# Optimization experiments

Hardware: AMD Instinct MI355X
Metric: run time of the kernel (lower is better)

Reference implementation:

```python
import jax, jax.numpy as jnp
import numpy as np

HEADS = 8
K = 3            # kernel_size per axis
RPB = 2 * K - 1  # rel-pos-bias extent per axis
EPS = 1e-5


def _nbr(dim, k):
    # NATTEN-style clamped window: shift window to stay fully inside [0, dim)
    q = jnp.arange(dim)
    start = jnp.clip(q - k // 2, 0, dim - k)
    nbr = start[:, None] + jnp.arange(k)[None, :]       # (dim, k) neighbor coords
    rel = nbr - q[:, None] + (k - 1)                    # (dim, k) in [0, 2k-2]
    return nbr, rel


def _instance_norm(x):
    # InstanceNorm3d, affine=False: normalize over spatial dims per (B, C)
    m = jnp.mean(x, axis=(2, 3, 4), keepdims=True)
    v = jnp.var(x, axis=(2, 3, 4), keepdims=True)
    return (x - m) * jax.lax.rsqrt(v + EPS)


def setup_inputs() -> dict:
    key = jax.random.key(0)
    ks = jax.random.split(key, 10)
    B, C, H, W, Z = 1, 128, 32, 32, 32
    Cf = 4 * C
    s = 0.02
    return {
        "x": jax.random.normal(ks[0], (B, C, H, W, Z), jnp.float32),
        "w_qkv": jax.random.normal(ks[1], (3 * C, C), jnp.float32) * s,
        "b_qkv": jnp.zeros((3 * C,), jnp.float32),
        "rpb": jax.random.normal(ks[2], (HEADS, RPB, RPB, RPB), jnp.float32) * s,
        "w_proj": jax.random.normal(ks[3], (C, C), jnp.float32) * s,
        "b_proj": jnp.zeros((C,), jnp.float32),
        "w_ffn1": jax.random.normal(ks[4], (Cf, C), jnp.float32) * s,
        "b_ffn1": jnp.zeros((Cf,), jnp.float32),
        "w_ffn2": jax.random.normal(ks[5], (C, Cf), jnp.float32) * s,
        "b_ffn2": jnp.zeros((C,), jnp.float32),
    }


def reference(x, w_qkv, b_qkv, rpb, w_proj, b_proj, w_ffn1, b_ffn1, w_ffn2, b_ffn2):
    B, C, H, W, Z = x.shape
    hd = C // HEADS
    N = H * W * Z
    KK = K ** 3

    # ---- SAM: 3D neighborhood self-attention ----
    xt = x.reshape(B, C, N).transpose(0, 2, 1)                 # (B, N, C)
    qkv = xt @ w_qkv.T + b_qkv                                  # (B, N, 3C)
    q, k_, v = jnp.split(qkv, 3, axis=-1)
    split = lambda t: t.reshape(B, N, HEADS, hd).transpose(0, 2, 1, 3)  # (B, h, N, d)
    q, k_, v = split(q), split(k_), split(v)

    nh, rh = _nbr(H, K)
    nw, rw = _nbr(W, K)
    nz, rz = _nbr(Z, K)
    # flat neighbor token index per (h, w, z, kh, kw, kz)
    nbr = ((nh[:, None, None, :, None, None] * W
            + nw[None, :, None, None, :, None]) * Z
           + nz[None, None, :, None, None, :]).reshape(N, KK)   # (N, 27)
    # flat rel-pos-bias index
    bidx = ((rh[:, None, None, :, None, None] * RPB
             + rw[None, :, None, None, :, None]) * RPB
            + rz[None, None, :, None, None, :]).reshape(N, KK)  # (N, 27)

    kg = k_[:, :, nbr]                                          # (B, h, N, 27, d)
    vg = v[:, :, nbr]                                           # (B, h, N, 27, d)
    bias = rpb.reshape(HEADS, RPB ** 3)[:, bidx]                # (h, N, 27)

    scale = jnp.asarray(hd, x.dtype) ** -0.5
    attn = jnp.einsum('bhnd,bhnkd->bhnk', q * scale, kg) + bias
    attn = jax.nn.softmax(attn, axis=-1)
    out = jnp.einsum('bhnk,bhnkd->bhnd', attn, vg)              # (B, h, N, d)
    out = out.transpose(0, 2, 1, 3).reshape(B, N, C) @ w_proj.T + b_proj
    x5 = out.transpose(0, 2, 1).reshape(B, C, H, W, Z)

    # ---- norm_in ----
    x5 = _instance_norm(x5)

    # ---- FFN (mmcv-style, GELU, residual identity) ----
    t = x5.reshape(B, C, N).transpose(0, 2, 1)                  # (B, N, C)
    t = t + (jax.nn.gelu(t @ w_ffn1.T + b_ffn1) @ w_ffn2.T + b_ffn2)
    x5 = t.transpose(0, 2, 1).reshape(B, C, H, W, Z)

    # ---- norm_out ----
    return _instance_norm(x5)
```

## Files before the change

kernel.cpp:

```cpp
#include <hip/hip_runtime.h>
#include <hip/hip_bf16.h>
#include <math.h>

#define NPOS 32768
#define CCH  128
#define C3   384
#define CF   512

typedef __attribute__((ext_vector_type(8))) short short8;
typedef __attribute__((ext_vector_type(4))) float f32x4;

__device__ inline float bf2f(unsigned short u) {
    union { unsigned int i; float f; } x; x.i = ((unsigned int)u) << 16; return x.f;
}
__device__ inline unsigned short f2bf(float f) {
    union { float f; unsigned int i; } x; x.f = f;
    unsigned int r = x.i + 0x7FFFu + ((x.i >> 16) & 1u);
    return (unsigned short)(r >> 16);
}
__device__ inline float lo_bf(unsigned int u) {
    union { unsigned int i; float f; } x; x.i = u << 16; return x.f;
}
__device__ inline float hi_bf(unsigned int u) {
    union { unsigned int i; float f; } x; x.i = u & 0xffff0000u; return x.f;
}

template<bool GELU, bool RES, bool WF32, bool WBF>
__global__ __launch_bounds__(256) void gemm_mfma(
    const unsigned short* __restrict__ A, const unsigned short* __restrict__ B,
    const float* __restrict__ bias, const unsigned short* __restrict__ res,
    float* __restrict__ outf, unsigned short* __restrict__ outb,
    int M, int Nout, int K)
{
    __shared__ alignas(16) unsigned short As[128 * 40];
    __shared__ alignas(16) unsigned short Bs[128 * 40];

    const int tid  = threadIdx.x;
    const int lane = tid & 63;
    const int wave = tid >> 6;
    const int wm = wave & 1, wn = wave >> 1;
    const int row0 = blockIdx.y * 128;
    const int col0 = blockIdx.x * 128;

    const f32x4 fzero = {0.f, 0.f, 0.f, 0.f};
    f32x4 acc[4][4];
    #pragma unroll
    for (int i = 0; i < 4; ++i)
        #pragma unroll
        for (int j = 0; j < 4; ++j) acc[i][j] = fzero;

    const int lr = lane & 15;
    const int lk = (lane >> 4) * 8;

    for (int kt = 0; kt < K; kt += 32) {
        #pragma unroll
        for (int it = 0; it < 2; ++it) {
            const int c = tid + it * 256;
            const int r = c >> 2;
            const int p = (c & 3) * 8;
            *(uint4*)&As[r * 40 + p] = *(const uint4*)&A[(size_t)(row0 + r) * K + kt + p];
            *(uint4*)&Bs[r * 40 + p] = *(const uint4*)&B[(size_t)(col0 + r) * K + kt + p];
        }
        __syncthreads();
        short8 af[4], bfr[4];
        #pragma unroll
        for (int i = 0; i < 4; ++i)
            af[i]  = *(const short8*)&As[(wm * 64 + i * 16 + lr) * 40 + lk];
        #pragma unroll
        for (int j = 0; j < 4; ++j)
            bfr[j] = *(const short8*)&Bs[(wn * 64 + j * 16 + lr) * 40 + lk];
        #pragma unroll
        for (int i = 0; i < 4; ++i)
            #pragma unroll
            for (int j = 0; j < 4; ++j)
                acc[i][j] = __builtin_amdgcn_mfma_f32_16x16x32_bf16(
                                af[i], bfr[j], acc[i][j], 0, 0, 0);
        __syncthreads();
    }

    const int gr0 = row0 + wm * 64 + (lane >> 4) * 4;
    const int gc0 = col0 + wn * 64 + lr;
    #pragma unroll
    for (int j = 0; j < 4; ++j) {
        const int gc = gc0 + j * 16;
        const float bv = bias[gc];
        #pragma unroll
        for (int i = 0; i < 4; ++i) {
            #pragma unroll
            for (int r = 0; r < 4; ++r) {
                const int gr = gr0 + i * 16 + r;
                float v = acc[i][j][r] + bv;
                if (GELU) {
                    const float g = 0.7978845608028654f * (v + 0.044715f * v * v * v);
                    const float e = __expf(2.f * g);
                    v = v * (e / (e + 1.f));
                }
                if (RES)  v += bf2f(res[(size_t)gr * Nout + gc]);
                if (WF32) outf[(size_t)gr * Nout + gc] = v;
                if (WBF)  outb[(size_t)gr * Nout + gc] = f2bf(v);
            }
        }
    }
}

__global__ __launch_bounds__(256) void attn_tiled(
    const unsigned short* __restrict__ qkv, const float* __restrict__ rpb,
    unsigned short* __restrict__ out)
{
    __shared__ unsigned int ksu[288 * 8];
    __shared__ unsigned int vsu[288 * 8];
    __shared__ unsigned int qsu[32 * 8];
    __shared__ float logits[32 * 29];
    __shared__ float rpbs[125];

    const int t  = threadIdx.x;
    const int line = ((blockIdx.x & 7) << 7) + (blockIdx.x >> 3);
    const int h  = blockIdx.y;
    const int w0 = line & 31, h0 = line >> 5;
    const int n0 = (h0 << 10) + (w0 << 5);
    const int sh0 = min(max(h0 - 1, 0), 29);
    const int sw0 = min(max(w0 - 1, 0), 29);
    const int rh_off = sh0 - h0 + 2;
    const int rw_off = sw0 - w0 + 2;

    if (t < 64) {
        const int pos = t >> 1, part = t & 1;
        const uint4 raw = *(const uint4*)&qkv[(size_t)(n0 + pos) * C3 + h * 16 + part * 8];
        *(uint4*)&qsu[pos * 8 + part * 4] = raw;
    } else if (t < 192) {
        const int i = t - 64;
        if (i < 125) rpbs[i] = rpb[h * 125 + i];
    }
    for (int c = t; c < 1152; c += 256) {
        const int p = c >> 2, part = c & 3;
        const int ihw = p >> 5, z = p & 31;
        const int ih = (ihw * 11) >> 5;
        const int iw = ihw - 3 * ih;
        const int n = ((sh0 + ih) << 10) + ((sw0 + iw) << 5) + z;
        const uint4 raw = *(const uint4*)&qkv[(size_t)n * C3 + CCH + (part >> 1) * CCH
                                              + h * 16 + (part & 1) * 8];
        unsigned int* d = ((part < 2) ? ksu : vsu) + p * 8 + (part & 1) * 4;
        *(uint4*)d = raw;
    }
    __syncthreads();

    {
        const int q = t >> 3, j = t & 7;
        const int sz = min(max(q - 1, 0), 29);
        const int rz_off = sz - q + 2;
        float qf[16];
        #pragma unroll
        for (int d2 = 0; d2 < 8; ++d2) {
            const unsigned int u = qsu[q * 8 + d2];
            qf[2 * d2] = lo_bf(u); qf[2 * d2 + 1] = hi_bf(u);
        }
        for (int kk = j; kk < 27; kk += 8) {
            const int ihw = kk / 3, dz = kk - 3 * ihw;
            const int ih = ihw / 3,  iw = ihw - 3 * ih;
            const int p = ihw * 32 + sz + dz;
            float a = 0.f;
            #pragma unroll
            for (int d2 = 0; d2 < 8; ++d2) {
                const unsigned int u = ksu[p * 8 + d2];
                a += qf[2 * d2] * lo_bf(u) + qf[2 * d2 + 1] * hi_bf(u);
            }
            const int bidx = ((ih + rh_off) * 5 + (iw + rw_off)) * 5 + (dz + rz_off);
            logits[q * 29 + kk] = a * 0.25f + rpbs[bidx];
        }
    }
    __syncthreads();

    if (t < 32) {
        float mx = -1e30f;
        #pragma unroll
        for (int kk = 0; kk < 27; ++kk) mx = fmaxf(mx, logits[t * 29 + kk]);
        float s = 0.f;
        #pragma unroll
        for (int kk = 0; kk < 27; ++kk) {
            const float e = __expf(logits[t * 29 + kk] - mx);
            logits[t * 29 + kk] = e; s += e;
        }
        const float inv = 1.f / s;
        #pragma unroll
        for (int kk = 0; kk < 27; ++kk) logits[t * 29 + kk] *= inv;
    }
    __syncthreads();

    {
        const int q = t >> 3, d2 = t & 7;
        const int sz = min(max(q - 1, 0), 29);
        float ax = 0.f, ay = 0.f;
        #pragma unroll
        for (int kk = 0; kk < 27; ++kk) {
            const int p = (kk / 3) * 32 + sz + (kk % 3);
            const float w = logits[q * 29 + kk];
            const unsigned int u = vsu[p * 8 + d2];
            ax += w * lo_bf(u); ay += w * hi_bf(u);
        }
        const unsigned int o = ((unsigned int)f2bf(ay) << 16) | (unsigned int)f2bf(ax);
        *(unsigned int*)&out[(size_t)(n0 + q) * CCH + h * 16 + d2 * 2] = o;
    }
}

__global__ __launch_bounds__(256) void proj_stats_kernel(
    const unsigned short* __restrict__ attnO,
    const unsigned short* __restrict__ wproj,
    const float* __restrict__ b_proj,
    unsigned short* __restrict__ x5b,
    float* __restrict__ stats)
{
    __shared__ alignas(16) unsigned short As[128 * 136];
    __shared__ alignas(16) unsigned short Bs[128 * 136];
    __shared__ float red[256];

    const int t    = threadIdx.x;
    const int lane = t & 63;
    const int wave = t >> 6;
    const int wm = wave & 1, wn = wave >> 1;
    const int lr = lane & 15;
    const int lg = lane >> 4;
    const int lk = lg * 8;
    const int n0 = blockIdx.x * 128;

    red[t] = 0.f;
    #pragma unroll
    for (int it = 0; it < 8; ++it) {
        const int idx = t + it * 256;
        const int row = idx >> 4, rem = (idx & 15) * 8;
        *(uint4*)&As[row * 136 + rem] = *(const uint4*)&attnO[(size_t)(n0 + row) * CCH + rem];
        *(uint4*)&Bs[row * 136 + rem] = *(const uint4*)&wproj[row * CCH + rem];
    }
    __syncthreads();

    const f32x4 fzero = {0.f, 0.f, 0.f, 0.f};
    f32x4 acc[4][4];
    #pragma unroll
    for (int i = 0; i < 4; ++i)
        #pragma unroll
        for (int j = 0; j < 4; ++j) acc[i][j] = fzero;

    #pragma unroll
    for (int ks = 0; ks < 4; ++ks) {
        short8 af[4], bfr[4];
        #pragma unroll
        for (int i = 0; i < 4; ++i)
            af[i]  = *(const short8*)&As[(wm * 64 + i * 16 + lr) * 136 + ks * 32 + lk];
        #pragma unroll
        for (int j = 0; j < 4; ++j)
            bfr[j] = *(const short8*)&Bs[(wn * 64 + j * 16 + lr) * 136 + ks * 32 + lk];
        #pragma unroll
        for (int i = 0; i < 4; ++i)
            #pragma unroll
            for (int j = 0; j < 4; ++j)
                acc[i][j] = __builtin_amdgcn_mfma_f32_16x16x32_bf16(
                                af[i], bfr[j], acc[i][j], 0, 0, 0);
    }

    #pragma unroll
    for (int j = 0; j < 4; ++j) {
        const int gc = wn * 64 + j * 16 + lr;
        const float bv = b_proj[gc];
        float s = 0.f, q = 0.f;
        #pragma unroll
        for (int i = 0; i < 4; ++i)
            #pragma unroll
            for (int r = 0; r < 4; ++r) {
                const int gr = wm * 64 + i * 16 + lg * 4 + r;
                const float v = acc[i][j][r] + bv;
                s += v; q += v * v;
                x5b[(size_t)(n0 + gr) * CCH + gc] = f2bf(v);
            }
        atomicAdd(&red[gc], s);
        atomicAdd(&red[128 + gc], q);
    }
    __syncthreads();
    if (t < 128) {
        atomicAdd(&stats[t],       red[t]);
        atomicAdd(&stats[128 + t], red[128 + t]);
    }
}

__global__ __launch_bounds__(256, 1) void ffn_fused_kernel(
    const unsigned short* __restrict__ x5b,
    const unsigned short* __restrict__ w1,
    const float* __restrict__ b1,
    const unsigned short* __restrict__ w2,
    const float* __restrict__ b2,
    float* __restrict__ stats,
    float* __restrict__ tT)
{
    __shared__ alignas(16) unsigned short pool[4 * 17408 + 1024];
    unsigned short* As  = pool;
    unsigned short* W1s = pool + 17408;
    unsigned short* W2s = pool + 2 * 17408;
    unsigned short* Hs  = pool + 3 * 17408;
    float* red = (float*)(pool + 4 * 17408);
    float* ms  = red + 256;
    float* rss = ms + 128;

    const int t    = threadIdx.x;
    const int lane = t & 63;
    const int wave = t >> 6;
    const int wm = wave & 1, wn = wave >> 1;
    const int lr = lane & 15;
    const int lg = lane >> 4;
    const int lk = lg * 8;
    const int n0 = blockIdx.x * 128;
    const float invN = 1.f / (float)NPOS;
    const f32x4 fzero = {0.f, 0.f, 0.f, 0.f};

    red[t] = 0.f;
    if (t < 128) {
        const float m = stats[t] * invN;
        const float v = stats[128 + t] * invN - m * m;
        ms[t]  = m;
        rss[t] = rsqrtf(v + 1e-5f);
    }
    uint4 pw1[8], pw2[8];
    #pragma unroll
    for (int it = 0; it < 8; ++it) {
        const int idx = t + it * 256;
        const int row = idx >> 4, rem = (idx & 15) * 8;
        pw1[it] = *(const uint4*)&w1[(size_t)row * CCH + rem];
        pw2[it] = *(const uint4*)&w2[(size_t)row * CF + rem];
    }
    __syncthreads();

    #pragma unroll
    for (int it = 0; it < 8; ++it) {
        const int idx = t + it * 256;
        const int row = idx >> 4, c0 = (idx & 15) * 8;
        uint4 raw = *(const uint4*)&x5b[(size_t)(n0 + row) * CCH + c0];
        unsigned int u[4] = {raw.x, raw.y, raw.z, raw.w};
        #pragma unroll
        for (int p = 0; p < 4; ++p) {
            const int c = c0 + 2 * p;
            const float a = (lo_bf(u[p]) - ms[c])     * rss[c];
            const float b = (hi_bf(u[p]) - ms[c + 1]) * rss[c + 1];
            u[p] = ((unsigned int)f2bf(b) << 16) | (unsigned int)f2bf(a);
        }
        uint4 w; w.x = u[0]; w.y = u[1]; w.z = u[2]; w.w = u[3];
        *(uint4*)&As[row * 136 + c0] = w;
    }

    f32x4 acc[4][4];
    #pragma unroll
    for (int i = 0; i < 4; ++i)
        #pragma unroll
        for (int j = 0; j < 4; ++j) acc[i][j] = fzero;

    #pragma unroll 1
    for (int cc = 0; cc < 4; ++cc) {
        #pragma unroll
        for (int it = 0; it < 8; ++it) {
            const int idx = t + it * 256;
            const int row = idx >> 4, rem = (idx & 15) * 8;
            *(uint4*)&W1s[row * 136 + rem] = pw1[it];
            *(uint4*)&W2s[row * 136 + rem] = pw2[it];
        }
        __syncthreads();
        if (cc < 3) {
            #pragma unroll
            for (int it = 0; it < 8; ++it) {
                const int idx = t + it * 256;
                const int row = idx >> 4, rem = (idx & 15) * 8;
                pw1[it] = *(const uint4*)&w1[(size_t)((cc + 1) * 128 + row) * CCH + rem];
                pw2[it] = *(const uint4*)&w2[(size_t)row * CF + (cc + 1) * 128 + rem];
            }
        }
        f32x4 hacc[4][4];
        #pragma unroll
        for (int i = 0; i < 4; ++i)
            #pragma unroll
            for (int j = 0; j < 4; ++j) hacc[i][j] = fzero;
        #pragma unroll
        for (int ks = 0; ks < 4; ++ks) {
            short8 af[4], bfr[4];
            #pragma unroll
            for (int i = 0; i < 4; ++i)
                af[i]  = *(const short8*)&As [(wm * 64 + i * 16 + lr) * 136 + ks * 32 + lk];
            #pragma unroll
            for (int j = 0; j < 4; ++j)
                bfr[j] = *(const short8*)&W1s[(wn * 64 + j * 16 + lr) * 136 + ks * 32 + lk];
            #pragma unroll
            for (int i = 0; i < 4; ++i)
                #pragma unroll
                for (int j = 0; j < 4; ++j)
                    hacc[i][j] = __builtin_amdgcn_mfma_f32_16x16x32_bf16(
                                    af[i], bfr[j], hacc[i][j], 0, 0, 0);
        }
        #pragma unroll
        for (int j = 0; j < 4; ++j) {
            const int gc = wn * 64 + j * 16 + lr;
            const float bv = b1[cc * 128 + gc];
            #pragma unroll
            for (int i = 0; i < 4; ++i)
                #pragma unroll
                for (int r = 0; r < 4; ++r) {
                    float v = hacc[i][j][r] + bv;
                    const float g = 0.7978845608028654f * (v + 0.044715f * v * v * v);
                    const float e = __expf(2.f * g);
                    v = v * (e / (e + 1.f));
                    const int gr = wm * 64 + i * 16 + lg * 4 + r;
                    Hs[gr * 136 + gc] = f2bf(v);
                }
        }
        __syncthreads();
        #pragma unroll
        for (int ks = 0; ks < 4; ++ks) {
            short8 af[4], bfr[4];
            #pragma unroll
            for (int i = 0; i < 4; ++i)
                af[i]  = *(const short8*)&Hs [(wm * 64 + i * 16 + lr) * 136 + ks * 32 + lk];
            #pragma unroll
            for (int j = 0; j < 4; ++j)
                bfr[j] = *(const short8*)&W2s[(wn * 64 + j * 16 + lr) * 136 + ks * 32 + lk];
            #pragma unroll
            for (int i = 0; i < 4; ++i)
                #pragma unroll
                for (int j = 0; j < 4; ++j)
                    acc[i][j] = __builtin_amdgcn_mfma_f32_16x16x32_bf16(
                                    af[i], bfr[j], acc[i][j], 0, 0, 0);
        }
        __syncthreads();
    }

    #pragma unroll
    for (int j = 0; j < 4; ++j) {
        const int gc = wn * 64 + j * 16 + lr;
        const float bv = b2[gc];
        float s = 0.f, q = 0.f;
        #pragma unroll
        for (int i = 0; i < 4; ++i)
            #pragma unroll
            for (int r = 0; r < 4; ++r) {
                const int gr = wm * 64 + i * 16 + lg * 4 + r;
                const float v = acc[i][j][r] + bv + bf2f(As[gr * 136 + gc]);
                acc[i][j][r] = v;
                s += v; q += v * v;
            }
        atomicAdd(&red[gc], s);
        atomicAdd(&red[128 + gc], q);
    }
    __syncthreads();
    if (t < 128) {
        atomicAdd(&stats[256 + t], red[t]);
        atomicAdd(&stats[384 + t], red[128 + t]);
    }
    __syncthreads();

    float* tr = (float*)(pool + 17408);
    #pragma unroll
    for (int j = 0; j < 4; ++j) {
        const int gc = wn * 64 + j * 16 + lr;
        #pragma unroll
        for (int i = 0; i < 4; ++i)
            #pragma unroll
            for (int r = 0; r < 4; ++r) {
                const int gr = wm * 64 + i * 16 + lg * 4 + r;
                tr[gc * 133 + gr] = acc[i][j][r];
            }
    }
    __syncthreads();
    #pragma unroll
    for (int it = 0; it < 16; ++it) {
        const int idx = t + it * 256;
        const int c = idx >> 5, ch = (idx & 31) * 4;
        float4 o4;
        o4.x = tr[c * 133 + ch + 0];
        o4.y = tr[c * 133 + ch + 1];
        o4.z = tr[c * 133 + ch + 2];
        o4.w = tr[c * 133 + ch + 3];
        *(float4*)&tT[(size_t)c * NPOS + n0 + ch] = o4;
    }
}

__global__ __launch_bounds__(256) void norm2_apply_kernel(
    const float* __restrict__ tT, const float* __restrict__ stats,
    float* __restrict__ out)
{
    const int i = blockIdx.x * 256 + threadIdx.x;
    const size_t o = (size_t)i * 4;
    const int c = (int)(o >> 15);
    const float invN = 1.f / (float)NPOS;
    const float m  = stats[256 + c] * invN;
    const float vr = stats[384 + c] * invN - m * m;
    const float rs = rsqrtf(vr + 1e-5f);
    float4 v = ((const float4*)tT)[i];
    v.x = (v.x - m) * rs;
    v.y = (v.y - m) * rs;
    v.z = (v.z - m) * rs;
    v.w = (v.w - m) * rs;
    ((float4*)out)[i] = v;
}

__global__ __launch_bounds__(256) void prep_kernel(
    const float* __restrict__ wq, const float* __restrict__ wp,
    const float* __restrict__ w1, const float* __restrict__ w2,
    unsigned short* __restrict__ wq_b, unsigned short* __restrict__ wp_b,
    unsigned short* __restrict__ w1_b, unsigned short* __restrict__ w2_b,
    float* __restrict__ stats)
{
    const int i = blockIdx.x * 256 + threadIdx.x;
    if (blockIdx.x == 0) {
        stats[threadIdx.x] = 0.f;
        stats[threadIdx.x + 256] = 0.f;
    }
    const float* src; unsigned short* dst; int off;
    if (i < 12288)      { src = wq; dst = wq_b; off = i; }
    else if (i < 16384) { src = wp; dst = wp_b; off = i - 12288; }
    else if (i < 32768) { src = w1; dst = w1_b; off = i - 16384; }
    else                { src = w2; dst = w2_b; off = i - 32768; }
    const float4 v = ((const float4*)src)[off];
    ushort4 o;
    o.x = f2bf(v.x); o.y = f2bf(v.y); o.z = f2bf(v.z); o.w = f2bf(v.w);
    ((ushort4*)dst)[off] = o;
}

__global__ __launch_bounds__(256) void transpose_x_kernel(
    const float* __restrict__ x, unsigned short* __restrict__ xt)
{
    __shared__ float tile[32][33];
    const int n0 = blockIdx.x * 32;
    const int c0 = blockIdx.y * 32;
    const int tx = threadIdx.x & 31;
    const int ty = threadIdx.x >> 5;
    for (int i = ty; i < 32; i += 8)
        tile[i][tx] = x[(size_t)(c0 + i) * NPOS + n0 + tx];
    __syncthreads();
    for (int i = ty; i < 32; i += 8)
        xt[(size_t)(n0 + i) * CCH + c0 + tx] = f2bf(tile[tx][i]);
}

extern "C" void kernel_launch(void* const* d_in, const int* in_sizes, int n_in,
                              void* d_out, int out_size, void* d_ws, size_t ws_size,
                              hipStream_t stream)
{
    const float* x      = (const float*)d_in[0];
    const float* w_qkv  = (const float*)d_in[1];
    const float* b_qkv  = (const float*)d_in[2];
    const float* rpb    = (const float*)d_in[3];
    const float* w_proj = (const float*)d_in[4];
    const float* b_proj = (const float*)d_in[5];
    const float* w_ffn1 = (const float*)d_in[6];
    const float* b_ffn1 = (const float*)d_in[7];
    const float* w_ffn2 = (const float*)d_in[8];
    const float* b_ffn2 = (const float*)d_in[9];
    float* out = (float*)d_out;

    char* ws = (char*)d_ws;
    unsigned short* xt_bf    = (unsigned short*)(ws + 0);
    unsigned short* qkv_bf   = (unsigned short*)(ws + 8388608);
    unsigned short* attnO_bf = (unsigned short*)(ws + 33554432);
    unsigned short* x5_bf    = (unsigned short*)(ws + 41943040);
    float*          tT       = (float*)(ws + 50331648);
    unsigned short* wqkv_bf  = (unsigned short*)(ws + 83886080);
    unsigned short* wproj_bf = (unsigned short*)(ws + 83984384);
    unsigned short* wffn1_bf = (unsigned short*)(ws + 84017152);
    unsigned short* wffn2_bf = (unsigned short*)(ws + 84148224);
    float*          stats    = (float*)(ws + 84279296);

    prep_kernel<<<192, 256, 0, stream>>>(w_qkv, w_proj, w_ffn1, w_ffn2,
                                         wqkv_bf, wproj_bf, wffn1_bf, wffn2_bf, stats);
    transpose_x_kernel<<<dim3(NPOS / 32, CCH / 32), 256, 0, stream>>>(x, xt_bf);

    gemm_mfma<false, false, false, true><<<dim3(C3 / 128, NPOS / 128), 256, 0, stream>>>(
        xt_bf, wqkv_bf, b_qkv, nullptr, nullptr, qkv_bf, NPOS, C3, CCH);

    attn_tiled<<<dim3(1024, 8), 256, 0, stream>>>(qkv_bf, rpb, attnO_bf);

    proj_stats_kernel<<<NPOS / 128, 256, 0, stream>>>(
        attnO_bf, wproj_bf, b_proj, x5_bf, stats);

    ffn_fused_kernel<<<NPOS / 128, 256, 0, stream>>>(
        x5_bf, wffn1_bf, b_ffn1, wffn2_bf, b_ffn2, stats, tT);

    norm2_apply_kernel<<<(NPOS * CCH / 4) / 256, 256, 0, stream>>>(tT, stats, out);
}
```

Before: 205.6 us.

## Halve row tiles in proj and FFN kernels, share one weight LDS buffer

Both the projection and the fused FFN kernel now process 64 tokens per block instead of 128, with four waves each covering 32 output columns, and launch twice as many blocks. The FFN kernel drops the separate W1/W2 shared buffers in favour of one buffer reused for both weights, with the W2 chunk prefetched into registers while W1 is consumed. This cuts LDS and register use to allow two blocks per CU and more blocks over the GPU. The cost is that weights are reloaded per block twice as often, each 64-row tile gets less MFMA reuse, and an extra barrier is added per chunk.

```diff
diff --git a/kernel.cpp b/kernel.cpp
--- a/kernel.cpp
+++ b/kernel.cpp
@@ -202,70 +202,74 @@
     }
 }
 
-__global__ __launch_bounds__(256) void proj_stats_kernel(
+__global__ __launch_bounds__(256, 2) void proj_stats_kernel(
     const unsigned short* __restrict__ attnO,
     const unsigned short* __restrict__ wproj,
     const float* __restrict__ b_proj,
     unsigned short* __restrict__ x5b,
     float* __restrict__ stats)
 {
-    __shared__ alignas(16) unsigned short As[128 * 136];
+    __shared__ alignas(16) unsigned short As[64 * 136];
     __shared__ alignas(16) unsigned short Bs[128 * 136];
     __shared__ float red[256];
 
     const int t    = threadIdx.x;
     const int lane = t & 63;
-    const int wave = t >> 6;
-    const int wm = wave & 1, wn = wave >> 1;
+    const int wn   = t >> 6;
     const int lr = lane & 15;
     const int lg = lane >> 4;
     const int lk = lg * 8;
-    const int n0 = blockIdx.x * 128;
+    const int n0 = blockIdx.x * 64;
 
     red[t] = 0.f;
+    #pragma unroll
+    for (int it = 0; it < 4; ++it) {
+        const int idx = t + it * 256;
+        const int row = idx >> 4, rem = (idx & 15) * 8;
+        *(uint4*)&As[row * 136 + rem] = *(const uint4*)&attnO[(size_t)(n0 + row) * CCH + rem];
+    }
     #pragma unroll
     for (int it = 0; it < 8; ++it) {
         const int idx = t + it * 256;
         const int row = idx >> 4, rem = (idx & 15) * 8;
-        *(uint4*)&As[row * 136 + rem] = *(const uint4*)&attnO[(size_t)(n0 + row) * CCH + rem];
         *(uint4*)&Bs[row * 136 + rem] = *(const uint4*)&wproj[row * CCH + rem];
     }
     __syncthreads();
 
     const f32x4 fzero = {0.f, 0.f, 0.f, 0.f};
-    f32x4 acc[4][4];
+    f32x4 acc[4][2];
     #pragma unroll
     for (int i = 0; i < 4; ++i)
         #pragma unroll
-        for (int j = 0; j < 4; ++j) acc[i][j] = fzero;
+        for (int j = 0; j < 2; ++j) acc[i][j] = fzero;
 
     #pragma unroll
     for (int ks = 0; ks < 4; ++ks) {
-        short8 af[4], bfr[4];
-        #pragma unroll
-        for (int i = 0; i < 4; ++i)
-            af[i]  = *(const short8*)&As[(wm * 64 + i * 16 + lr) * 136 + ks * 32 + lk];
-        #pragma unroll
-        for (int j = 0; j < 4; ++j)
-            bfr[j] = *(const short8*)&Bs[(wn * 64 + j * 16 + lr) * 136 + ks * 32 + lk];
-        #pragma unroll
-        for (int i = 0; i < 4; ++i)
-            #pragma unroll
-            for (int j = 0; j < 4; ++j)
+        short8 af[4], bfr[2];
+        #pragma unroll
+        for (int i = 0; i < 4; ++i)
+            af[i]  = *(const short8*)&As[(i * 16 + lr) * 136 + ks * 32 + lk];
+        #pragma unroll
+        for (int j = 0; j < 2; ++j)
+            bfr[j] = *(const short8*)&Bs[(wn * 32 + j * 16 + lr) * 136 + ks * 32 + lk];
+        #pragma unroll
+        for (int i = 0; i < 4; ++i)
+            #pragma unroll
+            for (int j = 0; j < 2; ++j)
                 acc[i][j] = __builtin_amdgcn_mfma_f32_16x16x32_bf16(
                                 af[i], bfr[j], acc[i][j], 0, 0, 0);
     }
 
     #pragma unroll
-    for (int j = 0; j < 4; ++j) {
-        const int gc = wn * 64 + j * 16 + lr;
+    for (int j = 0; j < 2; ++j) {
+        const int gc = wn * 32 + j * 16 + lr;
         const float bv = b_proj[gc];
         float s = 0.f, q = 0.f;
         #pragma unroll
         for (int i = 0; i < 4; ++i)
             #pragma unroll
             for (int r = 0; r < 4; ++r) {
-                const int gr = wm * 64 + i * 16 + lg * 4 + r;
+                const int gr = i * 16 + lg * 4 + r;
                 const float v = acc[i][j][r] + bv;
                 s += v; q += v * v;
                 x5b[(size_t)(n0 + gr) * CCH + gc] = f2bf(v);
@@ -280,7 +284,7 @@
     }
 }
 
-__global__ __launch_bounds__(256, 1) void ffn_fused_kernel(
+__global__ __launch_bounds__(256, 2) void ffn_fused_kernel(
     const unsigned short* __restrict__ x5b,
     const unsigned short* __restrict__ w1,
     const float* __restrict__ b1,
@@ -289,23 +293,20 @@
     float* __restrict__ stats,
     float* __restrict__ tT)
 {
-    __shared__ alignas(16) unsigned short pool[4 * 17408 + 1024];
-    unsigned short* As  = pool;
-    unsigned short* W1s = pool + 17408;
-    unsigned short* W2s = pool + 2 * 17408;
-    unsigned short* Hs  = pool + 3 * 17408;
-    float* red = (float*)(pool + 4 * 17408);
-    float* ms  = red + 256;
-    float* rss = ms + 128;
+    __shared__ alignas(16) unsigned short As[64 * 136];
+    __shared__ alignas(16) unsigned short Ws[128 * 136];
+    __shared__ alignas(16) unsigned short Hs[64 * 136];
+    __shared__ float red[256];
+    __shared__ float ms[128];
+    __shared__ float rss[128];
 
     const int t    = threadIdx.x;
     const int lane = t & 63;
-    const int wave = t >> 6;
-    const int wm = wave & 1, wn = wave >> 1;
+    const int wn   = t >> 6;
     const int lr = lane & 15;
     const int lg = lane >> 4;
     const int lk = lg * 8;
-    const int n0 = blockIdx.x * 128;
+    const int n0 = blockIdx.x * 64;
     const float invN = 1.f / (float)NPOS;
     const f32x4 fzero = {0.f, 0.f, 0.f, 0.f};
 
@@ -316,22 +317,27 @@
         ms[t]  = m;
         rss[t] = rsqrtf(v + 1e-5f);
     }
-    uint4 pw1[8], pw2[8];
+    uint4 pw[8];
     #pragma unroll
     for (int it = 0; it < 8; ++it) {
         const int idx = t + it * 256;
         const int row = idx >> 4, rem = (idx & 15) * 8;
-        pw1[it] = *(const uint4*)&w1[(size_t)row * CCH + rem];
-        pw2[it] = *(const uint4*)&w2[(size_t)row * CF + rem];
-    }
-    __syncthreads();
-
-    #pragma unroll
-    for (int it = 0; it < 8; ++it) {
+        pw[it] = *(const uint4*)&w1[(size_t)row * CCH + rem];
+    }
+    uint4 px[4];
+    #pragma unroll
+    for (int it = 0; it < 4; ++it) {
         const int idx = t + it * 256;
         const int row = idx >> 4, c0 = (idx & 15) * 8;
-        uint4 raw = *(const uint4*)&x5b[(size_t)(n0 + row) * CCH + c0];
-        unsigned int u[4] = {raw.x, raw.y, raw.z, raw.w};
+        px[it] = *(const uint4*)&x5b[(size_t)(n0 + row) * CCH + c0];
+    }
+    __syncthreads();
+
+    #pragma unroll
+    for (int it = 0; it < 4; ++it) {
+        const int idx = t + it * 256;
+        const int row = idx >> 4, c0 = (idx & 15) * 8;
+        unsigned int u[4] = {px[it].x, px[it].y, px[it].z, px[it].w};
         #pragma unroll
         for (int p = 0; p < 4; ++p) {
             const int c = c0 + 2 * p;
@@ -343,11 +349,11 @@
         *(uint4*)&As[row * 136 + c0] = w;
     }
 
-    f32x4 acc[4][4];
+    f32x4 acc[4][2];
     #pragma unroll
     for (int i = 0; i < 4; ++i)
         #pragma unroll
-        for (int j = 0; j < 4; ++j) acc[i][j] = fzero;
+        for (int j = 0; j < 2; ++j) acc[i][j] = fzero;
 
     #pragma unroll 1
     for (int cc = 0; cc < 4; ++cc) {
@@ -355,43 +361,40 @@
         for (int it = 0; it < 8; ++it) {
             const int idx = t + it * 256;
             const int row = idx >> 4, rem = (idx & 15) * 8;
-            *(uint4*)&W1s[row * 136 + rem] = pw1[it];
-            *(uint4*)&W2s[row * 136 + rem] = pw2[it];
+            *(uint4*)&Ws[row * 136 + rem] = pw[it];
+        }
+        #pragma unroll
+        for (int it = 0; it < 8; ++it) {
+            const int idx = t + it * 256;
+            const int row = idx >> 4, rem = (idx & 15) * 8;
+            pw[it] = *(const uint4*)&w2[(size_t)row * CF + cc * 128 + rem];
         }
         __syncthreads();
-        if (cc < 3) {
-            #pragma unroll
-            for (int it = 0; it < 8; ++it) {
-                const int idx = t + it * 256;
-                const int row = idx >> 4, rem = (idx & 15) * 8;
-                pw1[it] = *(const uint4*)&w1[(size_t)((cc + 1) * 128 + row) * CCH + rem];
-                pw2[it] = *(const uint4*)&w2[(size_t)row * CF + (cc + 1) * 128 + rem];
-            }
-        }
-        f32x4 hacc[4][4];
-        #pragma unroll
-        for (int i = 0; i < 4; ++i)
-            #pragma unroll
-            for (int j = 0; j < 4; ++j) hacc[i][j] = fzero;
+
+        f32x4 hacc[4][2];
+        #pragma unroll
+        for (int i = 0; i < 4; ++i)
+            #pragma unroll
+            for (int j = 0; j < 2; ++j) hacc[i][j] = fzero;
         #pragma unroll
         for (int ks = 0; ks < 4; ++ks) {
-            short8 af[4], bfr[4];
+            short8 af[4], bfr[2];
             #pragma unroll
             for (int i = 0; i < 4; ++i)
-                af[i]  = *(const short8*)&As [(wm * 64 + i * 16 + lr) * 136 + ks * 32 + lk];
-            #pragma unroll
-            for (int j = 0; j < 4; ++j)
-                bfr[j] = *(const short8*)&W1s[(wn * 64 + j * 16 + lr) * 136 + ks * 32 + lk];
+                af[i]  = *(const short8*)&As[(i * 16 + lr) * 136 + ks * 32 + lk];
+            #pragma unroll
+            for (int j = 0; j < 2; ++j)
+                bfr[j] = *(const short8*)&Ws[(wn * 32 + j * 16 + lr) * 136 + ks * 32 + lk];
             #pragma unroll
             for (int i = 0; i < 4; ++i)
                 #pragma unroll
-                for (int j = 0; j < 4; ++j)
+                for (int j = 0; j < 2; ++j)
                     hacc[i][j] = __builtin_amdgcn_mfma_f32_16x16x32_bf16(
                                     af[i], bfr[j], hacc[i][j], 0, 0, 0);
         }
         #pragma unroll
-        for (int j = 0; j < 4; ++j) {
-            const int gc = wn * 64 + j * 16 + lr;
+        for (int j = 0; j < 2; ++j) {
+            const int gc = wn * 32 + j * 16 + lr;
             const float bv = b1[cc * 128 + gc];
             #pragma unroll
             for (int i = 0; i < 4; ++i)
@@ -401,24 +404,40 @@
                     const float g = 0.7978845608028654f * (v + 0.044715f * v * v * v);
                     const float e = __expf(2.f * g);
                     v = v * (e / (e + 1.f));
-                    const int gr = wm * 64 + i * 16 + lg * 4 + r;
-                    Hs[gr * 136 + gc] = f2bf(v);
+                    Hs[(i * 16 + lg * 4 + r) * 136 + gc] = f2bf(v);
                 }
         }
         __syncthreads();
+
+        #pragma unroll
+        for (int it = 0; it < 8; ++it) {
+            const int idx = t + it * 256;
+            const int row = idx >> 4, rem = (idx & 15) * 8;
+            *(uint4*)&Ws[row * 136 + rem] = pw[it];
+        }
+        if (cc < 3) {
+            #pragma unroll
+            for (int it = 0; it < 8; ++it) {
+                const int idx = t + it * 256;
+                const int row = idx >> 4, rem = (idx & 15) * 8;
+                pw[it] = *(const uint4*)&w1[(size_t)((cc + 1) * 128 + row) * CCH + rem];
+            }
+        }
+        __syncthreads();
+
         #pragma unroll
         for (int ks = 0; ks < 4; ++ks) {
-            short8 af[4], bfr[4];
+            short8 af[4], bfr[2];
             #pragma unroll
             for (int i = 0; i < 4; ++i)
-                af[i]  = *(const short8*)&Hs [(wm * 64 + i * 16 + lr) * 136 + ks * 32 + lk];
-            #pragma unroll
-            for (int j = 0; j < 4; ++j)
-                bfr[j] = *(const short8*)&W2s[(wn * 64 + j * 16 + lr) * 136 + ks * 32 + lk];
+                af[i]  = *(const short8*)&Hs[(i * 16 + lr) * 136 + ks * 32 + lk];
+            #pragma unroll
+            for (int j = 0; j < 2; ++j)
+                bfr[j] = *(const short8*)&Ws[(wn * 32 + j * 16 + lr) * 136 + ks * 32 + lk];
             #pragma unroll
             for (int i = 0; i < 4; ++i)
                 #pragma unroll
-                for (int j = 0; j < 4; ++j)
+                for (int j = 0; j < 2; ++j)
                     acc[i][j] = __builtin_amdgcn_mfma_f32_16x16x32_bf16(
                                     af[i], bfr[j], acc[i][j], 0, 0, 0);
         }
@@ -426,15 +445,15 @@
     }
 
     #pragma unroll
-    for (int j = 0; j < 4; ++j) {
-        const int gc = wn * 64 + j * 16 + lr;
+    for (int j = 0; j < 2; ++j) {
+        const int gc = wn * 32 + j * 16 + lr;
         const float bv = b2[gc];
         float s = 0.f, q = 0.f;
         #pragma unroll
         for (int i = 0; i < 4; ++i)
             #pragma unroll
             for (int r = 0; r < 4; ++r) {
-                const int gr = wm * 64 + i * 16 + lg * 4 + r;
+                const int gr = i * 16 + lg * 4 + r;
                 const float v = acc[i][j][r] + bv + bf2f(As[gr * 136 + gc]);
                 acc[i][j][r] = v;
                 s += v; q += v * v;
@@ -447,30 +466,29 @@
         atomicAdd(&stats[256 + t], red[t]);
         atomicAdd(&stats[384 + t], red[128 + t]);
     }
-    __syncthreads();
-
-    float* tr = (float*)(pool + 17408);
-    #pragma unroll
-    for (int j = 0; j < 4; ++j) {
-        const int gc = wn * 64 + j * 16 + lr;
+
+    float* tr = (float*)Ws;
+    #pragma unroll
+    for (int j = 0; j < 2; ++j) {
+        const int gc = wn * 32 + j * 16 + lr;
         #pragma unroll
         for (int i = 0; i < 4; ++i)
             #pragma unroll
             for (int r = 0; r < 4; ++r) {
-                const int gr = wm * 64 + i * 16 + lg * 4 + r;
-                tr[gc * 133 + gr] = acc[i][j][r];
+                const int gr = i * 16 + lg * 4 + r;
+                tr[gc * 68 + gr] = acc[i][j][r];
             }
     }
     __syncthreads();
     #pragma unroll
-    for (int it = 0; it < 16; ++it) {
+    for (int it = 0; it < 8; ++it) {
         const int idx = t + it * 256;
-        const int c = idx >> 5, ch = (idx & 31) * 4;
+        const int c = idx >> 4, ch = (idx & 15) * 4;
         float4 o4;
-        o4.x = tr[c * 133 + ch + 0];
-        o4.y = tr[c * 133 + ch + 1];
-        o4.z = tr[c * 133 + ch + 2];
-        o4.w = tr[c * 133 + ch + 3];
+        o4.x = tr[c * 68 + ch + 0];
+        o4.y = tr[c * 68 + ch + 1];
+        o4.z = tr[c * 68 + ch + 2];
+        o4.w = tr[c * 68 + ch + 3];
         *(float4*)&tT[(size_t)c * NPOS + n0 + ch] = o4;
     }
 }
@@ -569,10 +587,10 @@
 
     attn_tiled<<<dim3(1024, 8), 256, 0, stream>>>(qkv_bf, rpb, attnO_bf);
 
-    proj_stats_kernel<<<NPOS / 128, 256, 0, stream>>>(
+    proj_stats_kernel<<<NPOS / 64, 256, 0, stream>>>(
         attnO_bf, wproj_bf, b_proj, x5_bf, stats);
 
-    ffn_fused_kernel<<<NPOS / 128, 256, 0, stream>>>(
+    ffn_fused_kernel<<<NPOS / 64, 256, 0, stream>>>(
         x5_bf, wffn1_bf, b_ffn1, wffn2_bf, b_ffn2, stats, tT);
 
     norm2_apply_kernel<<<(NPOS * CCH / 4) / 256, 256, 0, stream>>>(tT, stats, out);
```

Result: slower. 213.4 us (+3.8%).
